# Kernel optimization log

Measured on AMD Instinct MI355X. Metric: run time of the kernel, lower is better.

The kernel has to match this reference:

```python
import jax, jax.numpy as jnp
import numpy as np


def _expand_chunk(x):
    # prepend the previous bucket along the chunk axis: [b, nb, bl, ...] -> [b, nb, 2*bl, ...]
    return jnp.concatenate([jnp.roll(x, 1, axis=1), x], axis=2)


def _gather_seq(origin, idx):
    # origin [b, s, d], idx [b, s, r] -> out[b, s, :, r] = origin[b, idx[b, s, r], :]
    b = origin.shape[0]
    g = origin[jnp.arange(b)[:, None, None], idx]  # [b, s, r, d]
    return jnp.transpose(g, (0, 1, 3, 2))          # [b, s, d, r]


def _count_dup_keys(inp, rounds):
    # inp [b, s, K] int32: count duplicate key indices within a window of `rounds` in sorted order
    sort_idx = jnp.argsort(inp, axis=2)
    sorted_k = jnp.take_along_axis(inp, sort_idx, axis=2)
    unsort = jnp.argsort(sort_idx, axis=2)
    cnt = jnp.ones(inp.shape, jnp.float32)
    for i in range(1, rounds):
        eq = (sorted_k[..., i:] == sorted_k[..., :-i]).astype(jnp.float32)
        pad = jnp.zeros(inp.shape[:-1] + (i,), jnp.float32)
        cnt = cnt + jnp.concatenate([pad, eq], axis=-1) + jnp.concatenate([eq, pad], axis=-1)
    return jnp.take_along_axis(cnt, unsort, axis=2)


def setup_inputs() -> dict:
    key = jax.random.key(0)
    k1, k2, k3 = jax.random.split(key, 3)
    B_M_H, SEQ, D_K, N_ROUNDS, N_BUCKETS = 32, 2048, 64, 4, 32
    query = jax.random.normal(k1, (B_M_H, SEQ, D_K), jnp.float32)
    value = jax.random.normal(k2, (B_M_H, SEQ, D_K), jnp.float32)
    rand_matrix = jax.random.normal(k3, (B_M_H, D_K, N_ROUNDS, N_BUCKETS // 2), jnp.float32)
    return {"query": query, "value": value, "rand_matrix": rand_matrix}


def reference(query, value, rand_matrix):
    b, s, d = query.shape
    nr = rand_matrix.shape[2]
    n_buckets = 2 * rand_matrix.shape[3]
    bl = s // n_buckets  # bucket_len

    # --- LSH hashing: argmax over [proj, -proj], then make hashes unique per position ---
    proj = jnp.einsum('bsd,bdrk->bsrk', query, rand_matrix)
    hashes = jnp.argmax(jnp.concatenate([proj, -proj], axis=-1), axis=-1).astype(jnp.int32)
    hashes = hashes * s + jnp.arange(s, dtype=jnp.int32)[None, :, None]  # [b, s, nr]

    sort_idx = jnp.argsort(hashes, axis=1)      # [b, s, nr]
    unsort_idx = jnp.argsort(sort_idx, axis=1)  # [b, s, nr]

    # --- sort queries into buckets ---
    q = _gather_seq(query, sort_idx).reshape(b, n_buckets, bl, d, nr)
    k = _expand_chunk(q)  # [b, nb, 2*bl, d, nr]
    k = k * jax.lax.rsqrt(jnp.maximum(jnp.sum(k * k, axis=-2, keepdims=True), 1e-12))

    qk = jnp.einsum('bnidr,bnjdr->bnijr', q, k) / np.float32(np.sqrt(d))  # [b, nb, bl, 2bl, nr]

    # --- causal / self masks on original positions ---
    qi = sort_idx.reshape(b, n_buckets, bl, nr) % s
    ki = _expand_chunk(qi)  # [b, nb, 2bl, nr]
    mask1 = (qi[:, :, :, None, :] < ki[:, :, None, :, :]).astype(jnp.float32)
    mask2 = (qi[:, :, :, None, :] == ki[:, :, None, :, :]).astype(jnp.float32)
    qk = qk * (1 - mask1) + mask1 * (-1e9)
    qk = qk * (1 - mask2) + mask2 * (-1e5)

    # --- duplicate-key counting across rounds ---
    ki_b = jnp.broadcast_to(ki[:, :, None, :, :], (b, n_buckets, bl, 2 * bl, nr)).reshape(b, s, 2 * bl * nr)
    count_keys = _count_dup_keys(ki_b, nr).reshape(b, s, 2 * bl, nr)

    qk = qk.reshape(b, s, 2 * bl, nr)
    lse = jax.scipy.special.logsumexp(qk, axis=2)  # [b, s, nr]
    sm = jnp.exp(qk - lse[:, :, None, :]) / count_keys

    v = _gather_seq(value, sort_idx).reshape(b, n_buckets, bl, d, nr)
    vk = _expand_chunk(v)  # [b, nb, 2bl, d, nr]
    sm = sm.reshape(b, n_buckets, bl, 2 * bl, nr)
    att = jnp.einsum('bnijr,bnjdr->bnidr', sm, vk).reshape(b, s, d, nr)

    # --- unsort back to original order, per round ---
    att = jnp.transpose(att, (0, 1, 3, 2))  # [b, s, nr, d]
    att = jnp.take_along_axis(att, jnp.broadcast_to(unsort_idx[:, :, :, None], att.shape), axis=1)
    lse = jnp.take_along_axis(lse, unsort_idx, axis=1)

    # --- combine rounds weighted by softmax of logsumexp ---
    w = jax.nn.softmax(lse, axis=-1)  # [b, s, nr]
    return jnp.einsum('bsrd,bsr->bsd', att, w)
```

## Files before the change

kernel.cpp:

```cpp
#include <hip/hip_runtime.h>

typedef unsigned short u16;
typedef unsigned int   u32;
typedef short bf16x8 __attribute__((ext_vector_type(8)));
typedef float f32x16 __attribute__((ext_vector_type(16)));

#define S_  2048
#define D_  64
#define NR_ 4
#define NB_ 32

#define AS 72
#define VS 136
#define PS 136

#define LOG2E 1.44269504088896f
#define LN2   0.69314718055995f

__device__ __forceinline__ float ex2(float x){ return __builtin_amdgcn_exp2f(x); }
__device__ __forceinline__ float frcp(float x){ return __builtin_amdgcn_rcpf(x); }

__device__ __forceinline__ float bf2f(u16 u){ return __uint_as_float(((u32)u)<<16); }
__device__ __forceinline__ u16 f2bf(float f){
  u32 u = __float_as_uint(f);
  u32 r = (u + 0x7fffu + ((u>>16)&1u)) >> 16;
  return (u16)r;
}
__device__ __forceinline__ u32 pk2bf(float a, float b){
#if __has_builtin(__builtin_amdgcn_cvt_pk_bf16_f32)
  auto r = __builtin_amdgcn_cvt_pk_bf16_f32(a, b);
  u32 u; __builtin_memcpy(&u, &r, 4); return u;
#else
  return (u32)f2bf(a) | ((u32)f2bf(b) << 16);
#endif
}
__device__ __forceinline__ void unpack2(u32 w, float &a, float &b){
  a = __uint_as_float(w<<16);
  b = __uint_as_float(w & 0xffff0000u);
}
__device__ __forceinline__ bf16x8 ld8(const u16* p){
  union { uint4 u; bf16x8 v; } x;
  x.u = *(const uint4*)p;
  return x.v;
}

__global__ __launch_bounds__(256, 2) void k_hash(const float* __restrict__ q,
                                                 const float* __restrict__ v,
                                                 const float* __restrict__ R,
                                                 int* __restrict__ hout,
                                                 u16* __restrict__ qb,
                                                 u16* __restrict__ vbuf,
                                                 float* __restrict__ scq){
  __shared__ float Rl[4096];
  int b   = blockIdx.x >> 3;
  int pos = (blockIdx.x & 7) * 256 + threadIdx.x;

  {
    const float4* Rg = (const float4*)(R + (size_t)b * 4096);
    float4* Rs = (float4*)Rl;
    #pragma unroll
    for (int k = 0; k < 4; k++) Rs[k*256 + threadIdx.x] = Rg[k*256 + threadIdx.x];
  }
  __syncthreads();

  const float4* q4 = (const float4*)(q + ((size_t)b * S_ + pos) * D_);
  const float4* v4 = (const float4*)(v + ((size_t)b * S_ + pos) * D_);
  uint2* qw = (uint2*)(qb   + ((size_t)b * S_ + pos) * D_);
  uint2* vw = (uint2*)(vbuf + ((size_t)b * S_ + pos) * D_);

  float acc[64];
  #pragma unroll
  for (int i = 0; i < 64; i++) acc[i] = 0.f;
  float ss = 0.f;

  #pragma unroll 4
  for (int c = 0; c < 16; c++){
    float4 wa = q4[c];
    float4 xa = v4[c];
    ss += wa.x*wa.x + wa.y*wa.y + wa.z*wa.z + wa.w*wa.w;
    qw[c] = make_uint2(pk2bf(wa.x, wa.y), pk2bf(wa.z, wa.w));
    vw[c] = make_uint2(pk2bf(xa.x, xa.y), pk2bf(xa.z, xa.w));
    float qa[4] = {wa.x, wa.y, wa.z, wa.w};
    #pragma unroll
    for (int dd = 0; dd < 4; dd++){
      int d = c * 4 + dd;
      const float4* Rr = (const float4*)(&Rl[d * 64]);
      #pragma unroll
      for (int k4 = 0; k4 < 16; k4++){
        float4 rv = Rr[k4];
        acc[k4*4+0] += qa[dd] * rv.x;
        acc[k4*4+1] += qa[dd] * rv.y;
        acc[k4*4+2] += qa[dd] * rv.z;
        acc[k4*4+3] += qa[dd] * rv.w;
      }
    }
  }
  scq[(size_t)b * S_ + pos] = rsqrtf(fmaxf(ss, 1e-12f)) * 0.125f * LOG2E;

  #pragma unroll
  for (int r = 0; r < 4; r++){
    float bv = acc[r*16]; int bi = 0;
    #pragma unroll
    for (int m = 1; m < 32; m++){
      float vv = (m < 16) ? acc[r*16 + m] : -acc[r*16 + m - 16];
      if (vv > bv){ bv = vv; bi = m; }
    }
    hout[((size_t)b * NR_ + r) * S_ + pos] = bi;
  }
}

__global__ __launch_bounds__(256) void k_sort(const int* __restrict__ h,
                                              int* __restrict__ sidx,
                                              int* __restrict__ chk){
  __shared__ int cnt[32][257];
  __shared__ int base[32];
  int br = blockIdx.x;
  const int* hb = h + (size_t)br * S_;
  int t = threadIdx.x;

  #pragma unroll
  for (int hh = 0; hh < 32; hh++) cnt[hh][t] = 0;
  __syncthreads();

  int hv[8];
  const int4* hb4 = (const int4*)hb;
  int4 a0 = hb4[t*2], a1 = hb4[t*2+1];
  hv[0]=a0.x; hv[1]=a0.y; hv[2]=a0.z; hv[3]=a0.w;
  hv[4]=a1.x; hv[5]=a1.y; hv[6]=a1.z; hv[7]=a1.w;
  #pragma unroll
  for (int k = 0; k < 8; k++) cnt[hv[k]][t]++;
  __syncthreads();

  int wave = t >> 6, lane = t & 63;
  for (int hh = wave*8; hh < wave*8 + 8; hh++){
    int vals[4]; int s0 = 0;
    #pragma unroll
    for (int k = 0; k < 4; k++){ vals[k] = cnt[hh][lane*4+k]; s0 += vals[k]; }
    int incl = s0;
    #pragma unroll
    for (int off = 1; off < 64; off <<= 1){
      int o = __shfl_up(incl, off, 64);
      if (lane >= off) incl += o;
    }
    int run = incl - s0;
    #pragma unroll
    for (int k = 0; k < 4; k++){ int tmp = vals[k]; cnt[hh][lane*4+k] = run; run += tmp; }
    if (lane == 63) base[hh] = incl;
  }
  __syncthreads();
  if (t == 0){
    int run = 0;
    #pragma unroll
    for (int hh = 0; hh < 32; hh++){ int tot = base[hh]; base[hh] = run; run += tot; }
  }
  __syncthreads();

  int p0 = t * 8;
  #pragma unroll
  for (int k = 0; k < 8; k++){
    int hh = hv[k];
    int c = cnt[hh][t];
    int slot = base[hh] + c;
    cnt[hh][t] = c + 1;
    sidx[(size_t)br * S_ + slot]    = p0 + k;
    chk [(size_t)br * S_ + p0 + k]  = slot >> 6;
  }
}

__global__ __launch_bounds__(256, 4) void k_attn(const u16* __restrict__ qb,
                                                 const u16* __restrict__ vb,
                                                 const int* __restrict__ sidx,
                                                 const int* __restrict__ chk,
                                                 const float* __restrict__ scq,
                                                 float* __restrict__ lse_ws,
                                                 u16*  __restrict__ att_ws){
  __shared__ u16 A[128*AS];
  __shared__ u16 SM[64*PS];
  __shared__ int   pkey[128];
  __shared__ float rcnt[128];
  __shared__ float sc[128];
  __shared__ float pm[4*64];
  __shared__ float ps[4*64];

  int blk = blockIdx.x;
  int b = blk >> 7, r = (blk >> 5) & 3, n = blk & 31;
  int npv = (n + 31) & 31;
  int t = threadIdx.x;
  int lane = t & 63, w = t >> 6;
  int la = lane & 31, hh = lane >> 5;
  int coff = hh * 8;
  const int* sb = sidx + ((size_t)b * NR_ + r) * S_;

  int pmine = 0;
  if (t < 128){
    pmine = (t < 64) ? sb[npv*64 + t] : sb[n*64 + (t - 64)];
    pkey[t] = pmine;
  }
  __syncthreads();

  uint4 qk0, qk1, qk2, qk3;
  {
    int row = t >> 1, half = t & 1;
    const uint4* src = (const uint4*)(qb + ((size_t)b*S_ + pkey[row])*D_) + half*4;
    qk0 = src[0]; qk1 = src[1]; qk2 = src[2]; qk3 = src[3];
  }
  int jp = t & 63, dgrp = t >> 6;
  uint4 va0, va1, vb0, vb1;
  {
    const uint4* s0 = (const uint4*)(vb + ((size_t)b*S_ + pkey[2*jp  ])*D_ + dgrp*16);
    const uint4* s1 = (const uint4*)(vb + ((size_t)b*S_ + pkey[2*jp+1])*D_ + dgrp*16);
    va0 = s0[0]; va1 = s0[1]; vb0 = s1[0]; vb1 = s1[1];
  }
  if (t < 128){
    int c = 0;
    #pragma unroll
    for (int rr = 0; rr < 4; rr++){
      int ch = chk[((size_t)b * NR_ + rr) * S_ + pmine];
      c += (ch == n) || (ch == npv);
    }
    if (c < 1) c = 1;
    rcnt[t] = frcp((float)c);
    sc[t] = scq[(size_t)b * S_ + pmine];
  }
  {
    int row = t >> 1, half = t & 1;
    uint4* dst = (uint4*)(&A[row*AS + half*32]);
    dst[0] = qk0; dst[1] = qk1; dst[2] = qk2; dst[3] = qk3;
  }
  __syncthreads();

  float e0[16], e1[16];
  float ml0, ml1;
  {
    int jt = w;
    f32x16 acc0, acc1;
    #pragma unroll
    for (int i = 0; i < 16; i++){ acc0[i] = 0.f; acc1[i] = 0.f; }
    int arow  = (jt*32 + la) * AS;
    int brow0 = (64 + la) * AS;
    int brow1 = (96 + la) * AS;
    __builtin_amdgcn_s_setprio(1);
    #pragma unroll
    for (int ks = 0; ks < 4; ks++){
      int o = ks*16 + coff;
      bf16x8 af = ld8(&A[arow  + o]);
      bf16x8 b0 = ld8(&A[brow0 + o]);
      bf16x8 b1 = ld8(&A[brow1 + o]);
      acc0 = __builtin_amdgcn_mfma_f32_32x32x16_bf16(af, b0, acc0, 0, 0, 0);
      acc1 = __builtin_amdgcn_mfma_f32_32x32x16_bf16(af, b1, acc1, 0, 0, 0);
    }
    __builtin_amdgcn_s_setprio(0);
    int pj[16]; float scj[16];
    #pragma unroll
    for (int g = 0; g < 4; g++){
      int j0 = jt*32 + g*8 + 4*hh;
      int4   pv  = *(const int4*)(&pkey[j0]);
      float4 sv  = *(const float4*)(&sc[j0]);
      pj[g*4+0]=pv.x; pj[g*4+1]=pv.y; pj[g*4+2]=pv.z; pj[g*4+3]=pv.w;
      scj[g*4+0]=sv.x; scj[g*4+1]=sv.y; scj[g*4+2]=sv.z; scj[g*4+3]=sv.w;
    }
    int pi0 = pkey[64 + la], pi1 = pkey[96 + la];
    float x0[16], x1[16];
    #pragma unroll
    for (int reg = 0; reg < 16; reg++){
      float a0v = acc0[reg] * scj[reg];
      float a1v = acc1[reg] * scj[reg];
      if (pi0 < pj[reg]) a0v = -1442695040.0f; else if (pi0 == pj[reg]) a0v = -144269.504f;
      if (pi1 < pj[reg]) a1v = -1442695040.0f; else if (pi1 == pj[reg]) a1v = -144269.504f;
      x0[reg] = a0v; x1[reg] = a1v;
    }
    {
      float u0 = fmaxf(fmaxf(x0[0],x0[1]), fmaxf(x0[2],x0[3]));
      float u1 = fmaxf(fmaxf(x0[4],x0[5]), fmaxf(x0[6],x0[7]));
      float u2 = fmaxf(fmaxf(x0[8],x0[9]), fmaxf(x0[10],x0[11]));
      float u3 = fmaxf(fmaxf(x0[12],x0[13]), fmaxf(x0[14],x0[15]));
      ml0 = fmaxf(fmaxf(u0,u1), fmaxf(u2,u3));
      float w0 = fmaxf(fmaxf(x1[0],x1[1]), fmaxf(x1[2],x1[3]));
      float w1 = fmaxf(fmaxf(x1[4],x1[5]), fmaxf(x1[6],x1[7]));
      float w2 = fmaxf(fmaxf(x1[8],x1[9]), fmaxf(x1[10],x1[11]));
      float w3 = fmaxf(fmaxf(x1[12],x1[13]), fmaxf(x1[14],x1[15]));
      ml1 = fmaxf(fmaxf(w0,w1), fmaxf(w2,w3));
    }
    #pragma unroll
    for (int reg = 0; reg < 16; reg++){
      e0[reg] = ex2(x0[reg] - ml0);
      e1[reg] = ex2(x1[reg] - ml1);
    }
    float s0, s1;
    {
      float u0 = (e0[0]+e0[1])+(e0[2]+e0[3]);
      float u1 = (e0[4]+e0[5])+(e0[6]+e0[7]);
      float u2 = (e0[8]+e0[9])+(e0[10]+e0[11]);
      float u3 = (e0[12]+e0[13])+(e0[14]+e0[15]);
      s0 = (u0+u1)+(u2+u3);
      float w0 = (e1[0]+e1[1])+(e1[2]+e1[3]);
      float w1 = (e1[4]+e1[5])+(e1[6]+e1[7]);
      float w2 = (e1[8]+e1[9])+(e1[10]+e1[11]);
      float w3 = (e1[12]+e1[13])+(e1[14]+e1[15]);
      s1 = (w0+w1)+(w2+w3);
    }
    float om0 = __shfl_xor(ml0, 32, 64), os0 = __shfl_xor(s0, 32, 64);
    float om1 = __shfl_xor(ml1, 32, 64), os1 = __shfl_xor(s1, 32, 64);
    float m20 = fmaxf(ml0, om0);
    float m21 = fmaxf(ml1, om1);
    float s20 = s0 * ex2(ml0 - m20) + os0 * ex2(om0 - m20);
    float s21 = s1 * ex2(ml1 - m21) + os1 * ex2(om1 - m21);
    if (hh == 0){
      pm[jt*64 + la]      = m20;  ps[jt*64 + la]      = s20;
      pm[jt*64 + 32 + la] = m21;  ps[jt*64 + 32 + la] = s21;
    }
  }
  __syncthreads();

  {
    int jt = w;
    float mg0 = pm[la],      mg1 = pm[32 + la];
    #pragma unroll
    for (int k = 1; k < 4; k++){
      mg0 = fmaxf(mg0, pm[k*64 + la]);
      mg1 = fmaxf(mg1, pm[k*64 + 32 + la]);
    }
    float sg0 = 0.f, sg1 = 0.f;
    #pragma unroll
    for (int k = 0; k < 4; k++){
      sg0 += ps[k*64 + la]      * ex2(pm[k*64 + la]      - mg0);
      sg1 += ps[k*64 + 32 + la] * ex2(pm[k*64 + 32 + la] - mg1);
    }
    float f0 = ex2(ml0 - mg0) * frcp(sg0);
    float f1 = ex2(ml1 - mg1) * frcp(sg1);
    #pragma unroll
    for (int g = 0; g < 4; g++){
      int j0 = jt*32 + g*8 + 4*hh;
      float4 rc = *(const float4*)(&rcnt[j0]);
      float p00 = e0[g*4+0]*f0*rc.x, p01 = e0[g*4+1]*f0*rc.y;
      float p02 = e0[g*4+2]*f0*rc.z, p03 = e0[g*4+3]*f0*rc.w;
      float p10 = e1[g*4+0]*f1*rc.x, p11 = e1[g*4+1]*f1*rc.y;
      float p12 = e1[g*4+2]*f1*rc.z, p13 = e1[g*4+3]*f1*rc.w;
      *(uint2*)(&SM[la*PS + j0])        = make_uint2(pk2bf(p00,p01), pk2bf(p02,p03));
      *(uint2*)(&SM[(32+la)*PS + j0])   = make_uint2(pk2bf(p10,p11), pk2bf(p12,p13));
    }
    if (w == 0 && hh == 0){
      lse_ws[((size_t)b*S_ + pkey[64 + la])*NR_ + r] = mg0 * LN2 + __logf(sg0);
      lse_ws[((size_t)b*S_ + pkey[96 + la])*NR_ + r] = mg1 * LN2 + __logf(sg1);
    }
  }
  {
    u32 au[8] = {va0.x, va0.y, va0.z, va0.w, va1.x, va1.y, va1.z, va1.w};
    u32 bu[8] = {vb0.x, vb0.y, vb0.z, vb0.w, vb1.x, vb1.y, vb1.z, vb1.w};
    u32* vtp = (u32*)A;
    #pragma unroll
    for (int k = 0; k < 8; k++){
      int d0 = dgrp*16 + 2*k;
      u32 even = (au[k] & 0xffffu) | (bu[k] << 16);
      u32 odd  = (au[k] >> 16)     | (bu[k] & 0xffff0000u);
      vtp[ d0      * (VS/2) + jp] = even;
      vtp[(d0 + 1) * (VS/2) + jp] = odd;
    }
  }
  __syncthreads();

  {
    int Mt2 = w >> 1, Nt2 = w & 1;
    f32x16 acc;
    #pragma unroll
    for (int i = 0; i < 16; i++) acc[i] = 0.f;
    int arow = (Mt2*32 + la) * VS;
    int brow = (Nt2*32 + la) * PS;
    __builtin_amdgcn_s_setprio(1);
    #pragma unroll
    for (int ks = 0; ks < 8; ks++){
      int o = ks*16 + coff;
      bf16x8 af = ld8(&A[arow + o]);
      bf16x8 bf = ld8(&SM[brow + o]);
      acc = __builtin_amdgcn_mfma_f32_32x32x16_bf16(af, bf, acc, 0, 0, 0);
    }
    __builtin_amdgcn_s_setprio(0);
    int i = Nt2*32 + la;
    int p = pkey[64 + i];
    u16* base = att_ws + (((size_t)b*S_ + p)*NR_ + r)*D_ + Mt2*32 + 4*hh;
    #pragma unroll
    for (int g = 0; g < 4; g++){
      uint2 val = make_uint2(pk2bf(acc[4*g+0], acc[4*g+1]),
                             pk2bf(acc[4*g+2], acc[4*g+3]));
      *(uint2*)(base + g*8) = val;
    }
  }
}

__global__ __launch_bounds__(256) void k_comb(const float* __restrict__ lse_ws,
                                              const u16* __restrict__ att_ws,
                                              float* __restrict__ out){
  size_t idx4 = (size_t)blockIdx.x * 256 + threadIdx.x;
  size_t pd = idx4 >> 4;
  int d0 = (int)(idx4 & 15) * 4;
  float4 lv = *(const float4*)(lse_ws + pd * 4);
  float m = fmaxf(fmaxf(lv.x, lv.y), fmaxf(lv.z, lv.w));
  float e0 = __expf(lv.x - m), e1 = __expf(lv.y - m);
  float e2 = __expf(lv.z - m), e3 = __expf(lv.w - m);
  float inv = frcp(e0 + e1 + e2 + e3);
  e0 *= inv; e1 *= inv; e2 *= inv; e3 *= inv;
  const u16* a = att_ws + pd * 256 + d0;
  uint2 u0 = *(const uint2*)(a);
  uint2 u1 = *(const uint2*)(a + 64);
  uint2 u2 = *(const uint2*)(a + 128);
  uint2 u3 = *(const uint2*)(a + 192);
  float4 o;
  float a0,b0,a1,b1,a2,b2,a3,b3;
  unpack2(u0.x,a0,b0); unpack2(u1.x,a1,b1); unpack2(u2.x,a2,b2); unpack2(u3.x,a3,b3);
  o.x = a0*e0 + a1*e1 + a2*e2 + a3*e3;
  o.y = b0*e0 + b1*e1 + b2*e2 + b3*e3;
  unpack2(u0.y,a0,b0); unpack2(u1.y,a1,b1); unpack2(u2.y,a2,b2); unpack2(u3.y,a3,b3);
  o.z = a0*e0 + a1*e1 + a2*e2 + a3*e3;
  o.w = b0*e0 + b1*e1 + b2*e2 + b3*e3;
  *(float4*)(out + pd * D_ + d0) = o;
}

extern "C" void kernel_launch(void* const* d_in, const int* in_sizes, int n_in,
                              void* d_out, int out_size, void* d_ws, size_t ws_size,
                              hipStream_t stream){
  const float* q = (const float*)d_in[0];
  const float* v = (const float*)d_in[1];
  const float* R = (const float*)d_in[2];

  char* w = (char*)d_ws;
  int*   h    = (int*)  (w + 0);
  int*   sidx = (int*)  (w + (size_t)(1u << 20));
  int*   chkA = (int*)  (w + (size_t)(2u << 20));
  float* lse  = (float*)(w + (size_t)(3u << 20));
  u16*   att  = (u16*)  (w + (size_t)(4u << 20));
  u16*   qb   = (u16*)  (w + (size_t)(36u << 20));
  u16*   vbuf = (u16*)  (w + (size_t)(44u << 20));
  float* scq  = (float*)(w + (size_t)(52u << 20));
  float* out  = (float*)d_out;

  k_hash <<<256,  256, 0, stream>>>(q, v, R, h, qb, vbuf, scq);
  k_sort <<<128,  256, 0, stream>>>(h, sidx, chkA);
  k_attn <<<4096, 256, 0, stream>>>(qb, vbuf, sidx, chkA, scq, lse, att);
  k_comb <<<4096, 256, 0, stream>>>(lse, att, out);
}
```

Baseline: 153.7 us.

## Give each wave full key rows via 16x16 MFMA and defer softmax normalization

The QK^T stage now uses 16x16x32 MFMAs where each wave owns 16 query rows across all 128 keys, instead of each wave owning a 32-key slice of all 64 queries. Row max and sum are reduced inside the wave with shuffles, which removes the cross-wave pm/ps shared-memory exchange and one __syncthreads. Normalization by 1/sum is deferred: unnormalized exponentials go into SM and the PV output is scaled by a per-row reciprocal. Register pressure from 32 scores per lane and the larger number of MFMA issues may offset the savings.

Result: no change. 156.7 us (+2.0%).

```diff
diff --git a/kernel.cpp b/kernel.cpp
--- a/kernel.cpp
+++ b/kernel.cpp
@@ -4,6 +4,7 @@
 typedef unsigned int   u32;
 typedef short bf16x8 __attribute__((ext_vector_type(8)));
 typedef float f32x16 __attribute__((ext_vector_type(16)));
+typedef float f32x4  __attribute__((ext_vector_type(4)));
 
 #define S_  2048
 #define D_  64
@@ -179,8 +180,7 @@
   __shared__ int   pkey[128];
   __shared__ float rcnt[128];
   __shared__ float sc[128];
-  __shared__ float pm[4*64];
-  __shared__ float ps[4*64];
+  __shared__ float rsg[64];
 
   int blk = blockIdx.x;
   int b = blk >> 7, r = (blk >> 5) & 3, n = blk & 31;
@@ -188,6 +188,7 @@
   int t = threadIdx.x;
   int lane = t & 63, w = t >> 6;
   int la = lane & 31, hh = lane >> 5;
+  int la16 = lane & 15, g4 = lane >> 4;
   int coff = hh * 8;
   const int* sb = sidx + ((size_t)b * NR_ + r) * S_;
 
@@ -229,121 +230,75 @@
   }
   __syncthreads();
 
-  float e0[16], e1[16];
-  float ml0, ml1;
-  {
-    int jt = w;
-    f32x16 acc0, acc1;
-    #pragma unroll
-    for (int i = 0; i < 16; i++){ acc0[i] = 0.f; acc1[i] = 0.f; }
-    int arow  = (jt*32 + la) * AS;
-    int brow0 = (64 + la) * AS;
-    int brow1 = (96 + la) * AS;
+  {
+    int qrow = 64 + w*16;
+    f32x4 acc[8];
+    #pragma unroll
+    for (int jt = 0; jt < 8; jt++){ acc[jt][0]=0.f; acc[jt][1]=0.f; acc[jt][2]=0.f; acc[jt][3]=0.f; }
+    int aq = (qrow + la16) * AS + g4*8;
+    bf16x8 bq0 = ld8(&A[aq]);
+    bf16x8 bq1 = ld8(&A[aq + 32]);
     __builtin_amdgcn_s_setprio(1);
     #pragma unroll
-    for (int ks = 0; ks < 4; ks++){
-      int o = ks*16 + coff;
-      bf16x8 af = ld8(&A[arow  + o]);
-      bf16x8 b0 = ld8(&A[brow0 + o]);
-      bf16x8 b1 = ld8(&A[brow1 + o]);
-      acc0 = __builtin_amdgcn_mfma_f32_32x32x16_bf16(af, b0, acc0, 0, 0, 0);
-      acc1 = __builtin_amdgcn_mfma_f32_32x32x16_bf16(af, b1, acc1, 0, 0, 0);
+    for (int jt = 0; jt < 8; jt++){
+      int ak = (jt*16 + la16) * AS + g4*8;
+      bf16x8 a0 = ld8(&A[ak]);
+      bf16x8 a1 = ld8(&A[ak + 32]);
+      acc[jt] = __builtin_amdgcn_mfma_f32_16x16x32_bf16(a0, bq0, acc[jt], 0, 0, 0);
+      acc[jt] = __builtin_amdgcn_mfma_f32_16x16x32_bf16(a1, bq1, acc[jt], 0, 0, 0);
     }
     __builtin_amdgcn_s_setprio(0);
-    int pj[16]; float scj[16];
-    #pragma unroll
-    for (int g = 0; g < 4; g++){
-      int j0 = jt*32 + g*8 + 4*hh;
-      int4   pv  = *(const int4*)(&pkey[j0]);
-      float4 sv  = *(const float4*)(&sc[j0]);
-      pj[g*4+0]=pv.x; pj[g*4+1]=pv.y; pj[g*4+2]=pv.z; pj[g*4+3]=pv.w;
-      scj[g*4+0]=sv.x; scj[g*4+1]=sv.y; scj[g*4+2]=sv.z; scj[g*4+3]=sv.w;
-    }
-    int pi0 = pkey[64 + la], pi1 = pkey[96 + la];
-    float x0[16], x1[16];
-    #pragma unroll
-    for (int reg = 0; reg < 16; reg++){
-      float a0v = acc0[reg] * scj[reg];
-      float a1v = acc1[reg] * scj[reg];
-      if (pi0 < pj[reg]) a0v = -1442695040.0f; else if (pi0 == pj[reg]) a0v = -144269.504f;
-      if (pi1 < pj[reg]) a1v = -1442695040.0f; else if (pi1 == pj[reg]) a1v = -144269.504f;
-      x0[reg] = a0v; x1[reg] = a1v;
-    }
+
+    int pi = pkey[qrow + la16];
+    float x[32];
+    #pragma unroll
+    for (int jt = 0; jt < 8; jt++){
+      int j0 = jt*16 + g4*4;
+      int4   pv = *(const int4*)(&pkey[j0]);
+      float4 sv = *(const float4*)(&sc[j0]);
+      float x0 = acc[jt][0]*sv.x, x1 = acc[jt][1]*sv.y;
+      float x2 = acc[jt][2]*sv.z, x3 = acc[jt][3]*sv.w;
+      if (pi < pv.x) x0 = -1442695040.0f; else if (pi == pv.x) x0 = -144269.504f;
+      if (pi < pv.y) x1 = -1442695040.0f; else if (pi == pv.y) x1 = -144269.504f;
+      if (pi < pv.z) x2 = -1442695040.0f; else if (pi == pv.z) x2 = -144269.504f;
+      if (pi < pv.w) x3 = -1442695040.0f; else if (pi == pv.w) x3 = -144269.504f;
+      x[jt*4+0]=x0; x[jt*4+1]=x1; x[jt*4+2]=x2; x[jt*4+3]=x3;
+    }
+    float m;
     {
-      float u0 = fmaxf(fmaxf(x0[0],x0[1]), fmaxf(x0[2],x0[3]));
-      float u1 = fmaxf(fmaxf(x0[4],x0[5]), fmaxf(x0[6],x0[7]));
-      float u2 = fmaxf(fmaxf(x0[8],x0[9]), fmaxf(x0[10],x0[11]));
-      float u3 = fmaxf(fmaxf(x0[12],x0[13]), fmaxf(x0[14],x0[15]));
-      ml0 = fmaxf(fmaxf(u0,u1), fmaxf(u2,u3));
-      float w0 = fmaxf(fmaxf(x1[0],x1[1]), fmaxf(x1[2],x1[3]));
-      float w1 = fmaxf(fmaxf(x1[4],x1[5]), fmaxf(x1[6],x1[7]));
-      float w2 = fmaxf(fmaxf(x1[8],x1[9]), fmaxf(x1[10],x1[11]));
-      float w3 = fmaxf(fmaxf(x1[12],x1[13]), fmaxf(x1[14],x1[15]));
-      ml1 = fmaxf(fmaxf(w0,w1), fmaxf(w2,w3));
-    }
-    #pragma unroll
-    for (int reg = 0; reg < 16; reg++){
-      e0[reg] = ex2(x0[reg] - ml0);
-      e1[reg] = ex2(x1[reg] - ml1);
-    }
-    float s0, s1;
-    {
-      float u0 = (e0[0]+e0[1])+(e0[2]+e0[3]);
-      float u1 = (e0[4]+e0[5])+(e0[6]+e0[7]);
-      float u2 = (e0[8]+e0[9])+(e0[10]+e0[11]);
-      float u3 = (e0[12]+e0[13])+(e0[14]+e0[15]);
-      s0 = (u0+u1)+(u2+u3);
-      float w0 = (e1[0]+e1[1])+(e1[2]+e1[3]);
-      float w1 = (e1[4]+e1[5])+(e1[6]+e1[7]);
-      float w2 = (e1[8]+e1[9])+(e1[10]+e1[11]);
-      float w3 = (e1[12]+e1[13])+(e1[14]+e1[15]);
-      s1 = (w0+w1)+(w2+w3);
-    }
-    float om0 = __shfl_xor(ml0, 32, 64), os0 = __shfl_xor(s0, 32, 64);
-    float om1 = __shfl_xor(ml1, 32, 64), os1 = __shfl_xor(s1, 32, 64);
-    float m20 = fmaxf(ml0, om0);
-    float m21 = fmaxf(ml1, om1);
-    float s20 = s0 * ex2(ml0 - m20) + os0 * ex2(om0 - m20);
-    float s21 = s1 * ex2(ml1 - m21) + os1 * ex2(om1 - m21);
-    if (hh == 0){
-      pm[jt*64 + la]      = m20;  ps[jt*64 + la]      = s20;
-      pm[jt*64 + 32 + la] = m21;  ps[jt*64 + 32 + la] = s21;
-    }
-  }
-  __syncthreads();
-
-  {
-    int jt = w;
-    float mg0 = pm[la],      mg1 = pm[32 + la];
-    #pragma unroll
-    for (int k = 1; k < 4; k++){
-      mg0 = fmaxf(mg0, pm[k*64 + la]);
-      mg1 = fmaxf(mg1, pm[k*64 + 32 + la]);
-    }
-    float sg0 = 0.f, sg1 = 0.f;
-    #pragma unroll
-    for (int k = 0; k < 4; k++){
-      sg0 += ps[k*64 + la]      * ex2(pm[k*64 + la]      - mg0);
-      sg1 += ps[k*64 + 32 + la] * ex2(pm[k*64 + 32 + la] - mg1);
-    }
-    float f0 = ex2(ml0 - mg0) * frcp(sg0);
-    float f1 = ex2(ml1 - mg1) * frcp(sg1);
-    #pragma unroll
-    for (int g = 0; g < 4; g++){
-      int j0 = jt*32 + g*8 + 4*hh;
+      float u0 = fmaxf(fmaxf(x[0],x[1]), fmaxf(x[2],x[3]));
+      float u1 = fmaxf(fmaxf(x[4],x[5]), fmaxf(x[6],x[7]));
+      float u2 = fmaxf(fmaxf(x[8],x[9]), fmaxf(x[10],x[11]));
+      float u3 = fmaxf(fmaxf(x[12],x[13]), fmaxf(x[14],x[15]));
+      float u4 = fmaxf(fmaxf(x[16],x[17]), fmaxf(x[18],x[19]));
+      float u5 = fmaxf(fmaxf(x[20],x[21]), fmaxf(x[22],x[23]));
+      float u6 = fmaxf(fmaxf(x[24],x[25]), fmaxf(x[26],x[27]));
+      float u7 = fmaxf(fmaxf(x[28],x[29]), fmaxf(x[30],x[31]));
+      m = fmaxf(fmaxf(fmaxf(u0,u1), fmaxf(u2,u3)), fmaxf(fmaxf(u4,u5), fmaxf(u6,u7)));
+    }
+    m = fmaxf(m, __shfl_xor(m, 16, 64));
+    m = fmaxf(m, __shfl_xor(m, 32, 64));
+    float s = 0.f;
+    int srow = (w*16 + la16) * PS;
+    #pragma unroll
+    for (int jt = 0; jt < 8; jt++){
+      int j0 = jt*16 + g4*4;
       float4 rc = *(const float4*)(&rcnt[j0]);
-      float p00 = e0[g*4+0]*f0*rc.x, p01 = e0[g*4+1]*f0*rc.y;
-      float p02 = e0[g*4+2]*f0*rc.z, p03 = e0[g*4+3]*f0*rc.w;
-      float p10 = e1[g*4+0]*f1*rc.x, p11 = e1[g*4+1]*f1*rc.y;
-      float p12 = e1[g*4+2]*f1*rc.z, p13 = e1[g*4+3]*f1*rc.w;
-      *(uint2*)(&SM[la*PS + j0])        = make_uint2(pk2bf(p00,p01), pk2bf(p02,p03));
-      *(uint2*)(&SM[(32+la)*PS + j0])   = make_uint2(pk2bf(p10,p11), pk2bf(p12,p13));
-    }
-    if (w == 0 && hh == 0){
-      lse_ws[((size_t)b*S_ + pkey[64 + la])*NR_ + r] = mg0 * LN2 + __logf(sg0);
-      lse_ws[((size_t)b*S_ + pkey[96 + la])*NR_ + r] = mg1 * LN2 + __logf(sg1);
-    }
-  }
+      float e0v = ex2(x[jt*4+0] - m), e1v = ex2(x[jt*4+1] - m);
+      float e2v = ex2(x[jt*4+2] - m), e3v = ex2(x[jt*4+3] - m);
+      s += (e0v + e1v) + (e2v + e3v);
+      *(uint2*)(&SM[srow + j0]) = make_uint2(pk2bf(e0v*rc.x, e1v*rc.y),
+                                             pk2bf(e2v*rc.z, e3v*rc.w));
+    }
+    s += __shfl_xor(s, 16, 64);
+    s += __shfl_xor(s, 32, 64);
+    if (g4 == 0){
+      rsg[w*16 + la16] = frcp(s);
+      lse_ws[((size_t)b*S_ + pi)*NR_ + r] = m * LN2 + __logf(s);
+    }
+  }
+  __syncthreads();
+
   {
     u32 au[8] = {va0.x, va0.y, va0.z, va0.w, va1.x, va1.y, va1.z, va1.w};
     u32 bu[8] = {vb0.x, vb0.y, vb0.z, vb0.w, vb1.x, vb1.y, vb1.z, vb1.w};
@@ -376,12 +331,13 @@
     }
     __builtin_amdgcn_s_setprio(0);
     int i = Nt2*32 + la;
+    float rs = rsg[i];
     int p = pkey[64 + i];
     u16* base = att_ws + (((size_t)b*S_ + p)*NR_ + r)*D_ + Mt2*32 + 4*hh;
     #pragma unroll
     for (int g = 0; g < 4; g++){
-      uint2 val = make_uint2(pk2bf(acc[4*g+0], acc[4*g+1]),
-                             pk2bf(acc[4*g+2], acc[4*g+3]));
+      uint2 val = make_uint2(pk2bf(acc[4*g+0]*rs, acc[4*g+1]*rs),
+                             pk2bf(acc[4*g+2]*rs, acc[4*g+3]*rs));
       *(uint2*)(base + g*8) = val;
     }
   }
```
